# Kernel tuning notes

Measured on AMD Instinct MI355X. Metric: run time of the kernel, lower is better.

Reference implementation:

```python
import jax, jax.numpy as jnp
import numpy as np

TEMP = 0.07  # temperature used as logits / 0.07 in the original


def setup_inputs() -> dict:
    key = jax.random.key(0)
    k1, k2, k3 = jax.random.split(key, 3)
    B, N, T, L, D = 8, 128, 8, 6, 256
    meta = jax.random.normal(k1, (B, N, T, L, D), dtype=jnp.float32)
    thing = jax.random.randint(k2, (B, N, T), 0, 2, dtype=jnp.int32)
    label = jax.random.randint(k3, (B, N, T), 0, 40, dtype=jnp.int32)
    return {"meta_weight_for_con": meta, "thing_gt_idx": thing, "label_tmp": label}


def _con_loss(meta, thing, label):
    # meta: [B,N,T,L,D]; thing,label: [B,N,T]
    B, N, T, L, D = meta.shape
    P = N * T
    valid = thing.reshape(B, P).astype(bool)            # [B,P] boolean gt mask
    lab = label.reshape(B, P)                           # [B,P]
    # meta_weight_b[mask] -> [K,L,D]; permute(1,0,2) -> per-layer [K,D].
    # We keep all P positions and mask instead of compacting (jit-friendly).
    w = meta.reshape(B, P, L, D).transpose(0, 2, 1, 3)  # [B,L,P,D]
    w = w / jnp.maximum(jnp.linalg.norm(w, axis=-1, keepdims=True), 1e-12)  # F.normalize
    z = jnp.einsum('blpd,blqd->blpq', w, w) / TEMP      # similarity / temp [B,L,P,P]

    same = lab[:, :, None] == lab[:, None, :]           # [B,P,P]
    vpair = valid[:, :, None] & valid[:, None, :]
    eye = jnp.eye(P, dtype=bool)
    pos_mask = same & (~eye) & vpair                    # positives: same label, not self
    neg_mask = (~same) & vpair                          # negatives: different label

    K = valid.sum(axis=1)                               # [B] ins_num_ per batch
    pos_count = pos_mask.sum(axis=-1)                   # [B,P]
    neg_count = neg_mask.sum(axis=-1)                   # [B,P]

    # --- random positive sample per (batch, layer, row), mirroring np.random.choice ---
    u = jax.random.uniform(jax.random.key(42), (B, L, P))
    r = jnp.floor(u * pos_count[:, None, :].astype(u.dtype)).astype(jnp.int32)
    r = jnp.minimum(r, jnp.maximum(pos_count - 1, 0)[:, None, :])
    ranks = jnp.cumsum(pos_mask, axis=-1) - 1           # rank of each positive in index order
    sel = pos_mask[:, None, :, :] & (ranks[:, None, :, :] == r[..., None])  # [B,L,P,P]
    zp = jnp.sum(jnp.where(sel, z, 0.0), axis=-1)       # chosen positive logit [B,L,P]
    diag = jnp.diagonal(z, axis1=-2, axis2=-1)          # self-sim fallback when no positives
    zp = jnp.where((pos_count > 0)[:, None, :], zp, diag)

    # --- last negative (original pads by repeating the last negative to K-1) ---
    iota = jnp.arange(P)
    idx_last = jnp.max(jnp.where(neg_mask, iota[None, None, :], -1), axis=-1)  # [B,P]
    idx = jnp.broadcast_to(jnp.maximum(idx_last, 0)[:, None, :, None], (B, L, P, 1))
    zl = jnp.take_along_axis(z, idx, axis=-1)[..., 0]   # [B,L,P]

    # --- stable CE with label 0: loss = lse(logits) - zp ---
    max_n = jnp.max(jnp.where(neg_mask[:, None], z, -jnp.inf), axis=-1)  # [B,L,P]
    m = jnp.maximum(zp, max_n)
    m = jnp.where(jnp.isfinite(m), m, zp)
    sum_neg = jnp.sum(jnp.where(neg_mask[:, None], jnp.exp(z - m[..., None]), 0.0), axis=-1)
    pad = jnp.maximum((K[:, None] - 1 - neg_count), 0).astype(z.dtype)   # [B,P]
    pad_term = pad[:, None, :] * jnp.where((neg_count > 0)[:, None, :], jnp.exp(zl - m), 0.0)
    loss_row = m + jnp.log(jnp.exp(zp - m) + sum_neg + pad_term) - zp    # [B,L,P]

    row_w = valid.astype(z.dtype)
    mean_per = jnp.sum(loss_row * row_w[:, None, :], axis=-1) / jnp.maximum(K, 1)[:, None].astype(z.dtype)  # [B,L]

    gate = jnp.sum((thing.sum(axis=2) > 0), axis=1) >= 2  # skip batches with <2 gt rows
    return jnp.sum(jnp.where(gate[:, None], mean_per, 0.0))


def reference(meta_weight_for_con, thing_gt_idx, label_tmp):
    return _con_loss(meta_weight_for_con, thing_gt_idx, label_tmp)
```

## Files before the change

kernel.cpp:

```cpp
#include <hip/hip_runtime.h>
#include <stdint.h>

namespace {

constexpr int Bb = 8, Ll = 6, Dd = 256, Pp = 1024;
constexpr float SCALE_Y = 14.285714285714286f * 1.4426950408889634f;
constexpr float M0y = 21.0f;
constexpr float LN2f = 0.6931471805599453f;

typedef __attribute__((ext_vector_type(4))) float floatx4;

__device__ const int PAIRS[36] = {
  0x00,0x01,0x02,0x03,0x04,0x05,0x06,0x07,
  0x11,0x12,0x13,0x14,0x15,0x16,0x17,
  0x22,0x23,0x24,0x25,0x26,0x27,
  0x33,0x34,0x35,0x36,0x37,
  0x44,0x45,0x46,0x47,
  0x55,0x56,0x57,
  0x66,0x67,
  0x77
};

__device__ __forceinline__ void async16(const void* g, void* l) {
  __builtin_amdgcn_global_load_lds(
      (const __attribute__((address_space(1))) void*)g,
      (__attribute__((address_space(3))) void*)l, 16, 0, 0);
}

__device__ __forceinline__ uint32_t rotl32(uint32_t x, int n) {
  return (x << n) | (x >> (32 - n));
}
__device__ __forceinline__ void tf_round(uint32_t& x0, uint32_t& x1, int r) {
  x0 += x1; x1 = rotl32(x1, r); x1 ^= x0;
}
__device__ void threefry2x32(uint32_t x0, uint32_t x1, uint32_t& o0, uint32_t& o1) {
  const uint32_t k0 = 0u, k1 = 42u;
  const uint32_t k2 = k0 ^ k1 ^ 0x1BD11BDAu;
  x0 += k0; x1 += k1;
  tf_round(x0,x1,13); tf_round(x0,x1,15); tf_round(x0,x1,26); tf_round(x0,x1,6);
  x0 += k1; x1 += k2 + 1u;
  tf_round(x0,x1,17); tf_round(x0,x1,29); tf_round(x0,x1,16); tf_round(x0,x1,24);
  x0 += k2; x1 += k0 + 2u;
  tf_round(x0,x1,13); tf_round(x0,x1,15); tf_round(x0,x1,26); tf_round(x0,x1,6);
  x0 += k0; x1 += k1 + 3u;
  tf_round(x0,x1,17); tf_round(x0,x1,29); tf_round(x0,x1,16); tf_round(x0,x1,24);
  x0 += k1; x1 += k2 + 4u;
  tf_round(x0,x1,13); tf_round(x0,x1,15); tf_round(x0,x1,26); tf_round(x0,x1,6);
  x0 += k2; x1 += k0 + 5u;
  o0 = x0; o1 = x1;
}
__device__ float jax_u01(uint32_t idx) {
  const uint32_t HALF = (uint32_t)(Bb * Ll * Pp / 2);
  uint32_t o0, o1, bits;
  if (idx < HALF) { threefry2x32(idx, idx + HALF, o0, o1); bits = o0; }
  else            { threefry2x32(idx - HALF, idx, o0, o1); bits = o1; }
  return __uint_as_float((bits >> 9) | 0x3f800000u) - 1.0f;
}

__device__ __forceinline__ uint32_t fp8e4m3_rne(float x) {
  uint32_t u = __float_as_uint(x);
  const uint32_t s = (u >> 24) & 0x80u;
  u &= 0x7FFFFFFFu;
  uint32_t code;
  if (u < 0x3C800000u) {
    code = (uint32_t)__float2int_rn(__uint_as_float(u) * 512.0f);
  } else {
    const uint32_t r = (u + 0x7FFFFu + ((u >> 20) & 1u)) >> 20;
    code = r - (120u << 3);
  }
  return s | code;
}
__device__ __forceinline__ float fp8e4m3_tof(uint32_t c) {
  const uint32_t e = (c >> 3) & 15u, m = c & 7u;
  float mag;
  if (e) mag = __uint_as_float(((e + 120u) << 23) | (m << 20));
  else   mag = (float)m * 0.001953125f;
  return (c & 0x80u) ? -mag : mag;
}

__device__ __forceinline__ void fp8x4_dot(uint32_t a, uint32_t b, float& s) {
#if __has_builtin(__builtin_amdgcn_cvt_f32_fp8)
  s += __builtin_amdgcn_cvt_f32_fp8((int)a, 0) * __builtin_amdgcn_cvt_f32_fp8((int)b, 0);
  s += __builtin_amdgcn_cvt_f32_fp8((int)a, 1) * __builtin_amdgcn_cvt_f32_fp8((int)b, 1);
  s += __builtin_amdgcn_cvt_f32_fp8((int)a, 2) * __builtin_amdgcn_cvt_f32_fp8((int)b, 2);
  s += __builtin_amdgcn_cvt_f32_fp8((int)a, 3) * __builtin_amdgcn_cvt_f32_fp8((int)b, 3);
#else
  s += fp8e4m3_tof(a & 0xFF) * fp8e4m3_tof(b & 0xFF);
  s += fp8e4m3_tof((a >> 8) & 0xFF) * fp8e4m3_tof((b >> 8) & 0xFF);
  s += fp8e4m3_tof((a >> 16) & 0xFF) * fp8e4m3_tof((b >> 16) & 0xFF);
  s += fp8e4m3_tof((a >> 24) & 0xFF) * fp8e4m3_tof((b >> 24) & 0xFF);
#endif
}

constexpr int NB_NORM = Bb * Pp * Ll / 4;
constexpr int NB_ROW  = Bb * Pp / 4;

__global__ void prep_k(const float* __restrict__ meta, const int* __restrict__ thing,
                       const int* __restrict__ label, uint8_t* __restrict__ wn,
                       int* __restrict__ qpos, int* __restrict__ negc,
                       int* __restrict__ qidx, int* __restrict__ Kv,
                       int* __restrict__ gatev, float* __restrict__ rowsum_g,
                       int* __restrict__ cnt2, float* __restrict__ out) {
  __shared__ int sK[256], sG[256];
  const int bid = blockIdx.x, t = threadIdx.x;

  if (bid < NB_NORM) {
    const int wid = (bid * 256 + t) >> 6;
    const int lane = t & 63;
    const float4 v = *(const float4*)(meta + (size_t)wid * Dd + lane * 4);
    float ss = v.x * v.x + v.y * v.y + v.z * v.z + v.w * v.w;
    #pragma unroll
    for (int m = 32; m; m >>= 1) ss += __shfl_xor(ss, m, 64);
    const float inv = 1.0f / fmaxf(sqrtf(ss), 1e-12f);
    const int bp = wid / Ll, l = wid - bp * Ll;
    const int b = bp >> 10, p = bp & (Pp - 1);
    uint8_t* dst = wn + ((size_t)(b * Ll + l) * Pp + p) * Dd + lane * 4;
#if __has_builtin(__builtin_amdgcn_cvt_pk_fp8_f32)
    const int lo16 = __builtin_amdgcn_cvt_pk_fp8_f32(v.x * inv, v.y * inv, 0, false);
    const uint32_t packed =
        (uint32_t)__builtin_amdgcn_cvt_pk_fp8_f32(v.z * inv, v.w * inv, lo16, true);
#else
    const uint32_t packed = fp8e4m3_rne(v.x * inv)
                          | (fp8e4m3_rne(v.y * inv) << 8)
                          | (fp8e4m3_rne(v.z * inv) << 16)
                          | (fp8e4m3_rne(v.w * inv) << 24);
#endif
    *(uint32_t*)dst = packed;
    return;
  }
  if (bid < NB_NORM + NB_ROW) {
    const int wid = (bid - NB_NORM) * 4 + (t >> 6);
    const int lane = t & 63;
    const int b = wid >> 10, p = wid & (Pp - 1);
    const int* lab = label + b * Pp;
    const int* th  = thing + b * Pp;
    const int myLab = lab[p];
    const bool myValid = (th[p] != 0);

    uint32_t posbits = 0;
    int cnt[16];
    int pc = 0, nc = 0, last = -1;
    #pragma unroll
    for (int c = 0; c < 16; ++c) {
      const int q = c * 64 + lane;
      const int lq = lab[q];
      const bool vq = (th[q] != 0);
      const bool same = (lq == myLab);
      const bool pos = myValid && vq && same && (q != p);
      const bool neg = myValid && vq && !same;
      uint64_t bp2 = __ballot(pos);
      uint64_t bn = __ballot(neg);
      if (pos) posbits |= (1u << c);
      cnt[c] = __popcll(bp2);
      pc += cnt[c];
      nc += __popcll(bn);
      if (bn) last = c * 64 + 63 - __clzll(bn);
    }
    int qsel[Ll];
    #pragma unroll
    for (int l = 0; l < Ll; ++l) qsel[l] = p;
    if (pc > 0) {
      for (int l = 0; l < Ll; ++l) {
        const float u = jax_u01((uint32_t)((b * Ll + l) * Pp + p));
        int r = (int)floorf(u * (float)pc);
        r = min(r, pc - 1);
        int base = 0;
        for (int c = 0; c < 16; ++c) {
          if (r < base + cnt[c]) {
            const bool mine = (posbits >> c) & 1u;
            uint64_t bm = __ballot(mine);
            uint64_t ltmask = (lane == 0) ? 0ull : (~0ull >> (64 - lane));
            int myrank = __popcll(bm & ltmask);
            bool hit = mine && (base + myrank == r);
            uint64_t hb = __ballot(hit);
            qsel[l] = c * 64 + (int)__builtin_ctzll(hb);
            break;
          }
          base += cnt[c];
        }
      }
    }
    if (lane == 0) {
      negc[wid] = nc;
      qidx[wid] = (last < 0) ? 0 : last;
      #pragma unroll
      for (int l = 0; l < Ll; ++l) qpos[(b * Ll + l) * Pp + p] = qsel[l];
    }
    return;
  }
  if (bid < NB_NORM + NB_ROW + Bb) {
    const int b = bid - (NB_NORM + NB_ROW);
    int k = 0;
    for (int p = t; p < Pp; p += 256) k += (thing[b * Pp + p] != 0);
    int g = 0;
    if (t < 128) {
      int any = 0;
      for (int tt = 0; tt < 8; ++tt) any |= (thing[(b * 128 + t) * 8 + tt] != 0);
      g = any;
    }
    sK[t] = k; sG[t] = g;
    __syncthreads();
    for (int s = 128; s; s >>= 1) {
      if (t < s) { sK[t] += sK[t + s]; sG[t] += sG[t + s]; }
      __syncthreads();
    }
    if (t == 0) { Kv[b] = sK[0]; gatev[b] = (sG[0] >= 2) ? 1 : 0; }
    return;
  }
  if (bid < NB_NORM + NB_ROW + Bb + 48) {
    const int zb = bid - (NB_NORM + NB_ROW + Bb);
    const int idx = zb * 256 + t;
    *(float4*)(rowsum_g + idx * 4) = (float4){0.f, 0.f, 0.f, 0.f};
    if (zb == 0 && t < 192) { cnt2[t] = 0; cnt2[t + 192] = 0; }
    return;
  }
  if (t == 0) out[0] = 0.f;
}

__global__ __launch_bounds__(512)
void gemmfinal_k(const uint8_t* __restrict__ wn,
                 const int* __restrict__ thing, const int* __restrict__ label,
                 const int* __restrict__ qpos, const int* __restrict__ qidx,
                 const int* __restrict__ negc, const int* __restrict__ Kv,
                 const int* __restrict__ gatev, float* __restrict__ rowsum_g,
                 int* __restrict__ cnt2, float* __restrict__ out) {
  __shared__ __align__(16) uint8_t As[2 * 128 * 64];
  __shared__ __align__(16) uint8_t Bs[2 * 128 * 64];
  __shared__ int labp_s[128], valp_s[128], labq_s[128], valq_s[128];
  __shared__ float rowsum_lds[128], colsum_lds[128];
  __shared__ int fin_s[2];
  __shared__ float sb[512];

  const int t = threadIdx.x;
  const int bid = blockIdx.x;
  const int xcd = bid & 7;
  const int chunk = bid >> 3;
  const int bl = xcd + 8 * (chunk % 6);
  const int b = bl / Ll;
  const int pair = PAIRS[chunk / 6];
  const int pt = pair >> 4, qt = pair & 15;
  const bool diag = (pt == qt);
  const int p0 = pt * 128, q0 = qt * 128;
  const int blP = bl * Pp;

  if (t < 128) {
    labp_s[t] = label[b * Pp + p0 + t];
    valp_s[t] = thing[b * Pp + p0 + t];
    labq_s[t] = label[b * Pp + q0 + t];
    valq_s[t] = thing[b * Pp + q0 + t];
    rowsum_lds[t] = 0.f;
    colsum_lds[t] = 0.f;
  }

  const uint8_t* Wbl = wn + (size_t)bl * Pp * Dd;
  const int lane = t & 63;
  const int w = t >> 6;
  const int wr = w >> 2, wc = w & 3;
  const int cq = lane & 15, rq = lane >> 4;
  const int wbase16 = (t & ~63) * 16;

  floatx4 acc[4][2];
  #pragma unroll
  for (int i = 0; i < 4; ++i)
    #pragma unroll
    for (int j = 0; j < 2; ++j) acc[i][j] = (floatx4){0.f, 0.f, 0.f, 0.f};

  auto STAGE = [&](int bsel, int kt) {
    const int k0 = kt * 64;
    const int row = t >> 2, sp2 = t & 3;
    const int sl = sp2 ^ ((row >> 1) & 3);
    async16(Wbl + (size_t)(p0 + row) * Dd + k0 + sl * 16,
            As + bsel * 8192 + wbase16);
    if (!diag)
      async16(Wbl + (size_t)(q0 + row) * Dd + k0 + sl * 16,
              Bs + bsel * 8192 + wbase16);
  };

  STAGE(0, 0);
  __syncthreads();

  const uint8_t* Bbase0 = diag ? As : Bs;
  for (int kt = 0; kt < 4; ++kt) {
    const int bsel = kt & 1;
    if (kt < 3) STAGE(bsel ^ 1, kt + 1);
    const uint8_t* Ab = As + bsel * 8192;
    const uint8_t* Bb2 = Bbase0 + bsel * 8192;
    #pragma unroll
    for (int sub = 0; sub < 2; ++sub) {
      const int Lw = sub * 2 + (rq >> 1);
      const int off8 = (rq & 1) * 8;
      long long af[4], bfr[2];
      #pragma unroll
      for (int fi = 0; fi < 4; ++fi) {
        const int row = wr * 64 + fi * 16 + cq;
        af[fi] = *(const long long*)(Ab + row * 64 + (Lw ^ ((row >> 1) & 3)) * 16 + off8);
      }
      #pragma unroll
      for (int fj = 0; fj < 2; ++fj) {
        const int row = wc * 32 + fj * 16 + cq;
        bfr[fj] = *(const long long*)(Bb2 + row * 64 + (Lw ^ ((row >> 1) & 3)) * 16 + off8);
      }
      #pragma unroll
      for (int fi = 0; fi < 4; ++fi)
        #pragma unroll
        for (int fj = 0; fj < 2; ++fj)
          acc[fi][fj] = __builtin_amdgcn_mfma_f32_16x16x32_fp8_fp8(af[fi], bfr[fj],
                                                                   acc[fi][fj], 0, 0, 0);
    }
    __syncthreads();
  }

  int qlabv[2];
  float qvalf[2];
  float csum[2] = {0.f, 0.f};
  #pragma unroll
  for (int fj = 0; fj < 2; ++fj) {
    const int cl = wc * 32 + fj * 16 + cq;
    qlabv[fj] = labq_s[cl];
    qvalf[fj] = valq_s[cl] ? 1.f : 0.f;
  }
  #pragma unroll
  for (int fi = 0; fi < 4; ++fi) {
    #pragma unroll
    for (int reg = 0; reg < 4; ++reg) {
      const int rl = wr * 64 + fi * 16 + rq * 4 + reg;
      const int rlab = labp_s[rl];
      const float rvalf = valp_s[rl] ? 1.f : 0.f;
      float rsum = 0.f;
      #pragma unroll
      for (int fj = 0; fj < 2; ++fj) {
        const float e = exp2f(fmaf(acc[fi][fj][reg], SCALE_Y, -M0y));
        const float negm = (qlabv[fj] != rlab) ? (qvalf[fj] * rvalf) : 0.f;
        const float term = negm * e;
        rsum += term;
        csum[fj] += term;
      }
      rsum += __shfl_xor(rsum, 1); rsum += __shfl_xor(rsum, 2);
      rsum += __shfl_xor(rsum, 4); rsum += __shfl_xor(rsum, 8);
      if (cq == 0) atomicAdd(&rowsum_lds[rl], rsum);
    }
  }
  if (!diag) {
    #pragma unroll
    for (int fj = 0; fj < 2; ++fj) {
      float c = csum[fj];
      c += __shfl_xor(c, 16); c += __shfl_xor(c, 32);
      if (rq == 0) atomicAdd(&colsum_lds[wc * 32 + fj * 16 + cq], c);
    }
  }
  __syncthreads();
  if (t < 128) {
    atomicAdd(&rowsum_g[blP + p0 + t], rowsum_lds[t]);
    if (!diag) atomicAdd(&rowsum_g[blP + q0 + t], colsum_lds[t]);
  }
  __syncthreads();

  if (t == 0) {
    const int n1 = __hip_atomic_fetch_add(&cnt2[bl * 8 + pt], 1,
                                          __ATOMIC_RELAXED, __HIP_MEMORY_SCOPE_AGENT);
    fin_s[0] = (n1 == 7);
    int f1 = 0;
    if (!diag) {
      const int n2 = __hip_atomic_fetch_add(&cnt2[bl * 8 + qt], 1,
                                            __ATOMIC_RELAXED, __HIP_MEMORY_SCOPE_AGENT);
      f1 = (n2 == 7);
    }
    fin_s[1] = f1;
  }
  __syncthreads();

  float accl = 0.f;
  if ((fin_s[0] | fin_s[1]) && gatev[b]) {
    const int Kb = Kv[b];
    const float invK = 1.f / (float)max(Kb, 1);
    const int qtr = t & 3;
    const int rrow = t >> 2;
    #pragma unroll
    for (int fr = 0; fr < 2; ++fr) {
      if (!fin_s[fr]) continue;
      const int p = (fr ? qt : pt) * 128 + rrow;
      const int valid = thing[b * Pp + p];
      const int qp = qpos[blP + p];
      const int qi = qidx[b * Pp + p];
      const uint8_t* rp = Wbl + (size_t)p  * Dd + qtr * 64;
      const uint8_t* rq2 = Wbl + (size_t)qp * Dd + qtr * 64;
      const uint8_t* rx = Wbl + (size_t)qi * Dd + qtr * 64;
      float sp = 0.f, sl = 0.f;
      #pragma unroll
      for (int i = 0; i < 4; ++i) {
        const uint4 a4 = *(const uint4*)(rp + i * 16);
        const uint4 b4 = *(const uint4*)(rq2 + i * 16);
        const uint4 c4 = *(const uint4*)(rx + i * 16);
        fp8x4_dot(a4.x, b4.x, sp); fp8x4_dot(a4.y, b4.y, sp);
        fp8x4_dot(a4.z, b4.z, sp); fp8x4_dot(a4.w, b4.w, sp);
        fp8x4_dot(a4.x, c4.x, sl); fp8x4_dot(a4.y, c4.y, sl);
        fp8x4_dot(a4.z, c4.z, sl); fp8x4_dot(a4.w, c4.w, sl);
      }
      sp += __shfl_xor(sp, 1); sp += __shfl_xor(sp, 2);
      sl += __shfl_xor(sl, 1); sl += __shfl_xor(sl, 2);
      if (qtr == 0 && valid != 0) {
        const float yp = sp * SCALE_Y, yl = sl * SCALE_Y;
        const float rs = __hip_atomic_load(&rowsum_g[blP + p],
                                           __ATOMIC_RELAXED, __HIP_MEMORY_SCOPE_AGENT);
        const int nc = negc[b * Pp + p];
        const float pad = fmaxf((float)(Kb - 1 - nc), 0.f);
        const float tot = exp2f(yp - M0y) + rs + ((nc > 0) ? pad * exp2f(yl - M0y) : 0.f);
        accl += LN2f * (M0y + log2f(tot) - yp) * invK;
      }
    }
  }
  sb[t] = accl;
  __syncthreads();
  for (int s = 256; s; s >>= 1) {
    if (t < s) sb[t] += sb[t + s];
    __syncthreads();
  }
  if (t == 0 && sb[0] != 0.f) atomicAdd(out, sb[0]);
}

}

extern "C" void kernel_launch(void* const* d_in, const int* in_sizes, int n_in,
                              void* d_out, int out_size, void* d_ws, size_t ws_size,
                              hipStream_t stream) {
  const float* meta = (const float*)d_in[0];
  const int* thing  = (const int*)d_in[1];
  const int* label  = (const int*)d_in[2];
  float* out = (float*)d_out;

  char* ws = (char*)d_ws;
  size_t off = 0;
  uint8_t* wn = (uint8_t*)(ws + off); off += (size_t)Bb * Ll * Pp * Dd;
  int* qpos  = (int*)(ws + off); off += (size_t)Bb * Ll * Pp * 4;
  int* negc  = (int*)(ws + off); off += (size_t)Bb * Pp * 4;
  int* qidx  = (int*)(ws + off); off += (size_t)Bb * Pp * 4;
  int* Kv    = (int*)(ws + off); off += 64;
  int* gatev = (int*)(ws + off); off += 64;
  float* rowsum_g = (float*)(ws + off); off += (size_t)Bb * Ll * Pp * 4;
  int* cnt2  = (int*)(ws + off); off += 384 * 4;

  const int nb_prep = NB_NORM + NB_ROW + Bb + 48 + 1;
  prep_k<<<nb_prep, 256, 0, stream>>>(meta, thing, label, wn, qpos, negc, qidx,
                                      Kv, gatev, rowsum_g, cnt2, out);
  gemmfinal_k<<<8 * 6 * 36, 512, 0, stream>>>(wn, thing, label, qpos, qidx, negc,
                                              Kv, gatev, rowsum_g, cnt2, out);
}
```

Baseline: 146.4 us.

## Process two tiles per block and prefetch next tile during epilogue

Halves the gemmfinal grid to 864 blocks, so each block loops over two 128x128 similarity tiles. The first k-stage of the second tile is issued asynchronously before the first tile's exp/mask epilogue, to hide its load latency. The final block reduction is skipped when the block finished no rows. In exchange there are fewer blocks to spread over the CUs, plus the extra loop and register pressure.

```diff
diff --git a/kernel.cpp b/kernel.cpp
--- a/kernel.cpp
+++ b/kernel.cpp
@@ -4,6 +4,7 @@
 namespace {
 
 constexpr int Bb = 8, Ll = 6, Dd = 256, Pp = 1024;
+constexpr int GF_GRID = 864;
 constexpr float SCALE_Y = 14.285714285714286f * 1.4426950408889634f;
 constexpr float M0y = 21.0f;
 constexpr float LN2f = 0.6931471805599453f;
@@ -229,193 +230,215 @@
   __shared__ int labp_s[128], valp_s[128], labq_s[128], valq_s[128];
   __shared__ float rowsum_lds[128], colsum_lds[128];
   __shared__ int fin_s[2];
+  __shared__ int fin_any;
   __shared__ float sb[512];
 
   const int t = threadIdx.x;
   const int bid = blockIdx.x;
-  const int xcd = bid & 7;
-  const int chunk = bid >> 3;
-  const int bl = xcd + 8 * (chunk % 6);
-  const int b = bl / Ll;
-  const int pair = PAIRS[chunk / 6];
-  const int pt = pair >> 4, qt = pair & 15;
-  const bool diag = (pt == qt);
-  const int p0 = pt * 128, q0 = qt * 128;
-  const int blP = bl * Pp;
-
-  if (t < 128) {
-    labp_s[t] = label[b * Pp + p0 + t];
-    valp_s[t] = thing[b * Pp + p0 + t];
-    labq_s[t] = label[b * Pp + q0 + t];
-    valq_s[t] = thing[b * Pp + q0 + t];
-    rowsum_lds[t] = 0.f;
-    colsum_lds[t] = 0.f;
-  }
-
-  const uint8_t* Wbl = wn + (size_t)bl * Pp * Dd;
   const int lane = t & 63;
   const int w = t >> 6;
   const int wr = w >> 2, wc = w & 3;
   const int cq = lane & 15, rq = lane >> 4;
   const int wbase16 = (t & ~63) * 16;
 
-  floatx4 acc[4][2];
-  #pragma unroll
-  for (int i = 0; i < 4; ++i)
-    #pragma unroll
-    for (int j = 0; j < 2; ++j) acc[i][j] = (floatx4){0.f, 0.f, 0.f, 0.f};
-
-  auto STAGE = [&](int bsel, int kt) {
+  if (t == 0) fin_any = 0;
+
+  auto STG = [&](const uint8_t* W, int pp, int qq, bool dg, int bsel, int kt) {
     const int k0 = kt * 64;
     const int row = t >> 2, sp2 = t & 3;
     const int sl = sp2 ^ ((row >> 1) & 3);
-    async16(Wbl + (size_t)(p0 + row) * Dd + k0 + sl * 16,
+    async16(W + (size_t)(pp + row) * Dd + k0 + sl * 16,
             As + bsel * 8192 + wbase16);
-    if (!diag)
-      async16(Wbl + (size_t)(q0 + row) * Dd + k0 + sl * 16,
+    if (!dg)
+      async16(W + (size_t)(qq + row) * Dd + k0 + sl * 16,
               Bs + bsel * 8192 + wbase16);
   };
 
-  STAGE(0, 0);
+  float accl = 0.f;
+
+  for (int it = 0; it < 2; ++it) {
+    const int tile = bid + it * GF_GRID;
+    const int xcd = tile & 7;
+    const int chunk = tile >> 3;
+    const int bl = xcd + 8 * (chunk % 6);
+    const int b = bl / Ll;
+    const int pair = PAIRS[chunk / 6];
+    const int pt = pair >> 4, qt = pair & 15;
+    const bool diag = (pt == qt);
+    const int p0 = pt * 128, q0 = qt * 128;
+    const int blP = bl * Pp;
+    const uint8_t* Wbl = wn + (size_t)bl * Pp * Dd;
+
+    __syncthreads();
+    if (t < 128) {
+      labp_s[t] = label[b * Pp + p0 + t];
+      valp_s[t] = thing[b * Pp + p0 + t];
+      labq_s[t] = label[b * Pp + q0 + t];
+      valq_s[t] = thing[b * Pp + q0 + t];
+      rowsum_lds[t] = 0.f;
+      colsum_lds[t] = 0.f;
+    }
+
+    floatx4 acc[4][2];
+    #pragma unroll
+    for (int i = 0; i < 4; ++i)
+      #pragma unroll
+      for (int j = 0; j < 2; ++j) acc[i][j] = (floatx4){0.f, 0.f, 0.f, 0.f};
+
+    if (it == 0) STG(Wbl, p0, q0, diag, 0, 0);
+    __syncthreads();
+
+    const uint8_t* Bbase0 = diag ? As : Bs;
+    for (int kt = 0; kt < 4; ++kt) {
+      const int bsel = kt & 1;
+      if (kt < 3) STG(Wbl, p0, q0, diag, bsel ^ 1, kt + 1);
+      const uint8_t* Ab = As + bsel * 8192;
+      const uint8_t* Bb2 = Bbase0 + bsel * 8192;
+      #pragma unroll
+      for (int sub = 0; sub < 2; ++sub) {
+        const int Lw = sub * 2 + (rq >> 1);
+        const int off8 = (rq & 1) * 8;
+        long long af[4], bfr[2];
+        #pragma unroll
+        for (int fi = 0; fi < 4; ++fi) {
+          const int row = wr * 64 + fi * 16 + cq;
+          af[fi] = *(const long long*)(Ab + row * 64 + (Lw ^ ((row >> 1) & 3)) * 16 + off8);
+        }
+        #pragma unroll
+        for (int fj = 0; fj < 2; ++fj) {
+          const int row = wc * 32 + fj * 16 + cq;
+          bfr[fj] = *(const long long*)(Bb2 + row * 64 + (Lw ^ ((row >> 1) & 3)) * 16 + off8);
+        }
+        #pragma unroll
+        for (int fi = 0; fi < 4; ++fi)
+          #pragma unroll
+          for (int fj = 0; fj < 2; ++fj)
+            acc[fi][fj] = __builtin_amdgcn_mfma_f32_16x16x32_fp8_fp8(af[fi], bfr[fj],
+                                                                     acc[fi][fj], 0, 0, 0);
+      }
+      __syncthreads();
+    }
+
+    if (it == 0) {
+      const int tile1 = bid + GF_GRID;
+      const int chunk1 = tile1 >> 3;
+      const int bl1 = (tile1 & 7) + 8 * (chunk1 % 6);
+      const int pair1 = PAIRS[chunk1 / 6];
+      const int pt1 = pair1 >> 4, qt1 = pair1 & 15;
+      STG(wn + (size_t)bl1 * Pp * Dd, pt1 * 128, qt1 * 128, pt1 == qt1, 0, 0);
+    }
+
+    int qlabv[2];
+    float qvalf[2];
+    float csum[2] = {0.f, 0.f};
+    #pragma unroll
+    for (int fj = 0; fj < 2; ++fj) {
+      const int cl = wc * 32 + fj * 16 + cq;
+      qlabv[fj] = labq_s[cl];
+      qvalf[fj] = valq_s[cl] ? 1.f : 0.f;
+    }
+    #pragma unroll
+    for (int fi = 0; fi < 4; ++fi) {
+      #pragma unroll
+      for (int reg = 0; reg < 4; ++reg) {
+        const int rl = wr * 64 + fi * 16 + rq * 4 + reg;
+        const int rlab = labp_s[rl];
+        const float rvalf = valp_s[rl] ? 1.f : 0.f;
+        float rsum = 0.f;
+        #pragma unroll
+        for (int fj = 0; fj < 2; ++fj) {
+          const float e = exp2f(fmaf(acc[fi][fj][reg], SCALE_Y, -M0y));
+          const float negm = (qlabv[fj] != rlab) ? (qvalf[fj] * rvalf) : 0.f;
+          const float term = negm * e;
+          rsum += term;
+          csum[fj] += term;
+        }
+        rsum += __shfl_xor(rsum, 1); rsum += __shfl_xor(rsum, 2);
+        rsum += __shfl_xor(rsum, 4); rsum += __shfl_xor(rsum, 8);
+        if (cq == 0) atomicAdd(&rowsum_lds[rl], rsum);
+      }
+    }
+    if (!diag) {
+      #pragma unroll
+      for (int fj = 0; fj < 2; ++fj) {
+        float c = csum[fj];
+        c += __shfl_xor(c, 16); c += __shfl_xor(c, 32);
+        if (rq == 0) atomicAdd(&colsum_lds[wc * 32 + fj * 16 + cq], c);
+      }
+    }
+    __syncthreads();
+    if (t < 128) {
+      atomicAdd(&rowsum_g[blP + p0 + t], rowsum_lds[t]);
+      if (!diag) atomicAdd(&rowsum_g[blP + q0 + t], colsum_lds[t]);
+    }
+    __syncthreads();
+
+    if (t == 0) {
+      const int n1 = __hip_atomic_fetch_add(&cnt2[bl * 8 + pt], 1,
+                                            __ATOMIC_RELAXED, __HIP_MEMORY_SCOPE_AGENT);
+      fin_s[0] = (n1 == 7);
+      int f1 = 0;
+      if (!diag) {
+        const int n2 = __hip_atomic_fetch_add(&cnt2[bl * 8 + qt], 1,
+                                              __ATOMIC_RELAXED, __HIP_MEMORY_SCOPE_AGENT);
+        f1 = (n2 == 7);
+      }
+      fin_s[1] = f1;
+      if (fin_s[0] | f1) fin_any = 1;
+    }
+    __syncthreads();
+
+    if ((fin_s[0] | fin_s[1]) && gatev[b]) {
+      const int Kb = Kv[b];
+      const float invK = 1.f / (float)max(Kb, 1);
+      const int qtr = t & 3;
+      const int rrow = t >> 2;
+      #pragma unroll
+      for (int fr = 0; fr < 2; ++fr) {
+        if (!fin_s[fr]) continue;
+        const int p = (fr ? qt : pt) * 128 + rrow;
+        const int valid = thing[b * Pp + p];
+        const int qp = qpos[blP + p];
+        const int qi = qidx[b * Pp + p];
+        const uint8_t* rp = Wbl + (size_t)p  * Dd + qtr * 64;
+        const uint8_t* rq2 = Wbl + (size_t)qp * Dd + qtr * 64;
+        const uint8_t* rx = Wbl + (size_t)qi * Dd + qtr * 64;
+        float sp = 0.f, sl = 0.f;
+        #pragma unroll
+        for (int i = 0; i < 4; ++i) {
+          const uint4 a4 = *(const uint4*)(rp + i * 16);
+          const uint4 b4 = *(const uint4*)(rq2 + i * 16);
+          const uint4 c4 = *(const uint4*)(rx + i * 16);
+          fp8x4_dot(a4.x, b4.x, sp); fp8x4_dot(a4.y, b4.y, sp);
+          fp8x4_dot(a4.z, b4.z, sp); fp8x4_dot(a4.w, b4.w, sp);
+          fp8x4_dot(a4.x, c4.x, sl); fp8x4_dot(a4.y, c4.y, sl);
+          fp8x4_dot(a4.z, c4.z, sl); fp8x4_dot(a4.w, c4.w, sl);
+        }
+        sp += __shfl_xor(sp, 1); sp += __shfl_xor(sp, 2);
+        sl += __shfl_xor(sl, 1); sl += __shfl_xor(sl, 2);
+        if (qtr == 0 && valid != 0) {
+          const float yp = sp * SCALE_Y, yl = sl * SCALE_Y;
+          const float rs = __hip_atomic_load(&rowsum_g[blP + p],
+                                             __ATOMIC_RELAXED, __HIP_MEMORY_SCOPE_AGENT);
+          const int nc = negc[b * Pp + p];
+          const float pad = fmaxf((float)(Kb - 1 - nc), 0.f);
+          const float tot = exp2f(yp - M0y) + rs + ((nc > 0) ? pad * exp2f(yl - M0y) : 0.f);
+          accl += LN2f * (M0y + log2f(tot) - yp) * invK;
+        }
+      }
+    }
+  }
+
   __syncthreads();
-
-  const uint8_t* Bbase0 = diag ? As : Bs;
-  for (int kt = 0; kt < 4; ++kt) {
-    const int bsel = kt & 1;
-    if (kt < 3) STAGE(bsel ^ 1, kt + 1);
-    const uint8_t* Ab = As + bsel * 8192;
-    const uint8_t* Bb2 = Bbase0 + bsel * 8192;
-    #pragma unroll
-    for (int sub = 0; sub < 2; ++sub) {
-      const int Lw = sub * 2 + (rq >> 1);
-      const int off8 = (rq & 1) * 8;
-      long long af[4], bfr[2];
-      #pragma unroll
-      for (int fi = 0; fi < 4; ++fi) {
-        const int row = wr * 64 + fi * 16 + cq;
-        af[fi] = *(const long long*)(Ab + row * 64 + (Lw ^ ((row >> 1) & 3)) * 16 + off8);
-      }
-      #pragma unroll
-      for (int fj = 0; fj < 2; ++fj) {
-        const int row = wc * 32 + fj * 16 + cq;
-        bfr[fj] = *(const long long*)(Bb2 + row * 64 + (Lw ^ ((row >> 1) & 3)) * 16 + off8);
-      }
-      #pragma unroll
-      for (int fi = 0; fi < 4; ++fi)
-        #pragma unroll
-        for (int fj = 0; fj < 2; ++fj)
-          acc[fi][fj] = __builtin_amdgcn_mfma_f32_16x16x32_fp8_fp8(af[fi], bfr[fj],
-                                                                   acc[fi][fj], 0, 0, 0);
-    }
-    __syncthreads();
-  }
-
-  int qlabv[2];
-  float qvalf[2];
-  float csum[2] = {0.f, 0.f};
-  #pragma unroll
-  for (int fj = 0; fj < 2; ++fj) {
-    const int cl = wc * 32 + fj * 16 + cq;
-    qlabv[fj] = labq_s[cl];
-    qvalf[fj] = valq_s[cl] ? 1.f : 0.f;
-  }
-  #pragma unroll
-  for (int fi = 0; fi < 4; ++fi) {
-    #pragma unroll
-    for (int reg = 0; reg < 4; ++reg) {
-      const int rl = wr * 64 + fi * 16 + rq * 4 + reg;
-      const int rlab = labp_s[rl];
-      const float rvalf = valp_s[rl] ? 1.f : 0.f;
-      float rsum = 0.f;
-      #pragma unroll
-      for (int fj = 0; fj < 2; ++fj) {
-        const float e = exp2f(fmaf(acc[fi][fj][reg], SCALE_Y, -M0y));
-        const float negm = (qlabv[fj] != rlab) ? (qvalf[fj] * rvalf) : 0.f;
-        const float term = negm * e;
-        rsum += term;
-        csum[fj] += term;
-      }
-      rsum += __shfl_xor(rsum, 1); rsum += __shfl_xor(rsum, 2);
-      rsum += __shfl_xor(rsum, 4); rsum += __shfl_xor(rsum, 8);
-      if (cq == 0) atomicAdd(&rowsum_lds[rl], rsum);
-    }
-  }
-  if (!diag) {
-    #pragma unroll
-    for (int fj = 0; fj < 2; ++fj) {
-      float c = csum[fj];
-      c += __shfl_xor(c, 16); c += __shfl_xor(c, 32);
-      if (rq == 0) atomicAdd(&colsum_lds[wc * 32 + fj * 16 + cq], c);
-    }
-  }
-  __syncthreads();
-  if (t < 128) {
-    atomicAdd(&rowsum_g[blP + p0 + t], rowsum_lds[t]);
-    if (!diag) atomicAdd(&rowsum_g[blP + q0 + t], colsum_lds[t]);
-  }
-  __syncthreads();
-
-  if (t == 0) {
-    const int n1 = __hip_atomic_fetch_add(&cnt2[bl * 8 + pt], 1,
-                                          __ATOMIC_RELAXED, __HIP_MEMORY_SCOPE_AGENT);
-    fin_s[0] = (n1 == 7);
-    int f1 = 0;
-    if (!diag) {
-      const int n2 = __hip_atomic_fetch_add(&cnt2[bl * 8 + qt], 1,
-                                            __ATOMIC_RELAXED, __HIP_MEMORY_SCOPE_AGENT);
-      f1 = (n2 == 7);
-    }
-    fin_s[1] = f1;
-  }
-  __syncthreads();
-
-  float accl = 0.f;
-  if ((fin_s[0] | fin_s[1]) && gatev[b]) {
-    const int Kb = Kv[b];
-    const float invK = 1.f / (float)max(Kb, 1);
-    const int qtr = t & 3;
-    const int rrow = t >> 2;
-    #pragma unroll
-    for (int fr = 0; fr < 2; ++fr) {
-      if (!fin_s[fr]) continue;
-      const int p = (fr ? qt : pt) * 128 + rrow;
-      const int valid = thing[b * Pp + p];
-      const int qp = qpos[blP + p];
-      const int qi = qidx[b * Pp + p];
-      const uint8_t* rp = Wbl + (size_t)p  * Dd + qtr * 64;
-      const uint8_t* rq2 = Wbl + (size_t)qp * Dd + qtr * 64;
-      const uint8_t* rx = Wbl + (size_t)qi * Dd + qtr * 64;
-      float sp = 0.f, sl = 0.f;
-      #pragma unroll
-      for (int i = 0; i < 4; ++i) {
-        const uint4 a4 = *(const uint4*)(rp + i * 16);
-        const uint4 b4 = *(const uint4*)(rq2 + i * 16);
-        const uint4 c4 = *(const uint4*)(rx + i * 16);
-        fp8x4_dot(a4.x, b4.x, sp); fp8x4_dot(a4.y, b4.y, sp);
-        fp8x4_dot(a4.z, b4.z, sp); fp8x4_dot(a4.w, b4.w, sp);
-        fp8x4_dot(a4.x, c4.x, sl); fp8x4_dot(a4.y, c4.y, sl);
-        fp8x4_dot(a4.z, c4.z, sl); fp8x4_dot(a4.w, c4.w, sl);
-      }
-      sp += __shfl_xor(sp, 1); sp += __shfl_xor(sp, 2);
-      sl += __shfl_xor(sl, 1); sl += __shfl_xor(sl, 2);
-      if (qtr == 0 && valid != 0) {
-        const float yp = sp * SCALE_Y, yl = sl * SCALE_Y;
-        const float rs = __hip_atomic_load(&rowsum_g[blP + p],
-                                           __ATOMIC_RELAXED, __HIP_MEMORY_SCOPE_AGENT);
-        const int nc = negc[b * Pp + p];
-        const float pad = fmaxf((float)(Kb - 1 - nc), 0.f);
-        const float tot = exp2f(yp - M0y) + rs + ((nc > 0) ? pad * exp2f(yl - M0y) : 0.f);
-        accl += LN2f * (M0y + log2f(tot) - yp) * invK;
-      }
-    }
-  }
-  sb[t] = accl;
-  __syncthreads();
-  for (int s = 256; s; s >>= 1) {
-    if (t < s) sb[t] += sb[t + s];
-    __syncthreads();
-  }
-  if (t == 0 && sb[0] != 0.f) atomicAdd(out, sb[0]);
+  if (fin_any) {
+    sb[t] = accl;
+    __syncthreads();
+    for (int s = 256; s; s >>= 1) {
+      if (t < s) sb[t] += sb[t + s];
+      __syncthreads();
+    }
+    if (t == 0 && sb[0] != 0.f) atomicAdd(out, sb[0]);
+  }
 }
 
 }
@@ -442,6 +465,6 @@
   const int nb_prep = NB_NORM + NB_ROW + Bb + 48 + 1;
   prep_k<<<nb_prep, 256, 0, stream>>>(meta, thing, label, wn, qpos, negc, qidx,
                                       Kv, gatev, rowsum_g, cnt2, out);
-  gemmfinal_k<<<8 * 6 * 36, 512, 0, stream>>>(wn, thing, label, qpos, qidx, negc,
-                                              Kv, gatev, rowsum_g, cnt2, out);
-}
+  gemmfinal_k<<<GF_GRID, 512, 0, stream>>>(wn, thing, label, qpos, qidx, negc,
+                                           Kv, gatev, rowsum_g, cnt2, out);
+}
```

Result: slower. 150.1 us (+2.5%).

## Load full K-depth tiles into LDS at once and exit early for non-final blocks

Applied to the files above, without the earlier changes.

Replaces the double-buffered 4-step K loop, with a sync after each step, by a single bulk async load of the whole 128x256 fp8 A and B tiles into LDS. The swizzle is adapted to 256-byte rows, and the MFMA loop then runs over all 8 sub-steps after one barrier. This removes per-step barriers and staging overhead. In exchange, LDS use grows from 32KB to 64KB per block, which may lower occupancy, and no compute overlaps with the loads. Blocks that are not the last one to finish their row tile now also return early before the finalize section.

```diff
diff --git a/kernel.cpp b/kernel.cpp
--- a/kernel.cpp
+++ b/kernel.cpp
@@ -224,11 +224,12 @@
                  const int* __restrict__ negc, const int* __restrict__ Kv,
                  const int* __restrict__ gatev, float* __restrict__ rowsum_g,
                  int* __restrict__ cnt2, float* __restrict__ out) {
-  __shared__ __align__(16) uint8_t As[2 * 128 * 64];
-  __shared__ __align__(16) uint8_t Bs[2 * 128 * 64];
+  __shared__ __align__(16) uint8_t As[128 * 256];
+  __shared__ __align__(16) uint8_t Bs[128 * 256];
   __shared__ int labp_s[128], valp_s[128], labq_s[128], valq_s[128];
   __shared__ float rowsum_lds[128], colsum_lds[128];
   __shared__ int fin_s[2];
+  __shared__ int fin_any;
   __shared__ float sb[512];
 
   const int t = threadIdx.x;
@@ -243,6 +244,7 @@
   const int p0 = pt * 128, q0 = qt * 128;
   const int blP = bl * Pp;
 
+  if (t == 0) fin_any = 0;
   if (t < 128) {
     labp_s[t] = label[b * Pp + p0 + t];
     valp_s[t] = thing[b * Pp + p0 + t];
@@ -259,55 +261,46 @@
   const int cq = lane & 15, rq = lane >> 4;
   const int wbase16 = (t & ~63) * 16;
 
+  #pragma unroll
+  for (int i = 0; i < 4; ++i) {
+    const int c = i * 512 + t;
+    const int row = c >> 4, sp = c & 15;
+    const int sl = sp ^ (row & 15);
+    async16(Wbl + (size_t)(p0 + row) * Dd + sl * 16, As + i * 8192 + wbase16);
+    if (!diag)
+      async16(Wbl + (size_t)(q0 + row) * Dd + sl * 16, Bs + i * 8192 + wbase16);
+  }
+
   floatx4 acc[4][2];
   #pragma unroll
   for (int i = 0; i < 4; ++i)
     #pragma unroll
     for (int j = 0; j < 2; ++j) acc[i][j] = (floatx4){0.f, 0.f, 0.f, 0.f};
 
-  auto STAGE = [&](int bsel, int kt) {
-    const int k0 = kt * 64;
-    const int row = t >> 2, sp2 = t & 3;
-    const int sl = sp2 ^ ((row >> 1) & 3);
-    async16(Wbl + (size_t)(p0 + row) * Dd + k0 + sl * 16,
-            As + bsel * 8192 + wbase16);
-    if (!diag)
-      async16(Wbl + (size_t)(q0 + row) * Dd + k0 + sl * 16,
-              Bs + bsel * 8192 + wbase16);
-  };
-
-  STAGE(0, 0);
   __syncthreads();
 
-  const uint8_t* Bbase0 = diag ? As : Bs;
-  for (int kt = 0; kt < 4; ++kt) {
-    const int bsel = kt & 1;
-    if (kt < 3) STAGE(bsel ^ 1, kt + 1);
-    const uint8_t* Ab = As + bsel * 8192;
-    const uint8_t* Bb2 = Bbase0 + bsel * 8192;
-    #pragma unroll
-    for (int sub = 0; sub < 2; ++sub) {
-      const int Lw = sub * 2 + (rq >> 1);
-      const int off8 = (rq & 1) * 8;
-      long long af[4], bfr[2];
+  const uint8_t* Bb2 = diag ? As : Bs;
+  #pragma unroll
+  for (int sub = 0; sub < 8; ++sub) {
+    const int Lw = sub * 2 + (rq >> 1);
+    const int off8 = (rq & 1) * 8;
+    long long af[4], bfr[2];
+    #pragma unroll
+    for (int fi = 0; fi < 4; ++fi) {
+      const int row = wr * 64 + fi * 16 + cq;
+      af[fi] = *(const long long*)(As + row * 256 + (Lw ^ (row & 15)) * 16 + off8);
+    }
+    #pragma unroll
+    for (int fj = 0; fj < 2; ++fj) {
+      const int row = wc * 32 + fj * 16 + cq;
+      bfr[fj] = *(const long long*)(Bb2 + row * 256 + (Lw ^ (row & 15)) * 16 + off8);
+    }
+    #pragma unroll
+    for (int fi = 0; fi < 4; ++fi)
       #pragma unroll
-      for (int fi = 0; fi < 4; ++fi) {
-        const int row = wr * 64 + fi * 16 + cq;
-        af[fi] = *(const long long*)(Ab + row * 64 + (Lw ^ ((row >> 1) & 3)) * 16 + off8);
-      }
-      #pragma unroll
-      for (int fj = 0; fj < 2; ++fj) {
-        const int row = wc * 32 + fj * 16 + cq;
-        bfr[fj] = *(const long long*)(Bb2 + row * 64 + (Lw ^ ((row >> 1) & 3)) * 16 + off8);
-      }
-      #pragma unroll
-      for (int fi = 0; fi < 4; ++fi)
-        #pragma unroll
-        for (int fj = 0; fj < 2; ++fj)
-          acc[fi][fj] = __builtin_amdgcn_mfma_f32_16x16x32_fp8_fp8(af[fi], bfr[fj],
-                                                                   acc[fi][fj], 0, 0, 0);
-    }
-    __syncthreads();
+      for (int fj = 0; fj < 2; ++fj)
+        acc[fi][fj] = __builtin_amdgcn_mfma_f32_16x16x32_fp8_fp8(af[fi], bfr[fj],
+                                                                 acc[fi][fj], 0, 0, 0);
   }
 
   int qlabv[2];
@@ -366,11 +359,14 @@
       f1 = (n2 == 7);
     }
     fin_s[1] = f1;
+    if (fin_s[0] | f1) fin_any = 1;
   }
   __syncthreads();
 
+  if (!fin_any) return;
+
   float accl = 0.f;
-  if ((fin_s[0] | fin_s[1]) && gatev[b]) {
+  if (gatev[b]) {
     const int Kb = Kv[b];
     const float invK = 1.f / (float)max(Kb, 1);
     const int qtr = t & 3;
```

After: 159.4 us. +8.9%, slower.
